# Performance work log

Measured on AMD Instinct MI355X. Metric: run time of the kernel, lower is better.

The kernel has to match this reference:

```python
import jax, jax.numpy as jnp
import numpy as np

L, B, N, D, H = 2, 4, 2048, 1024, 16
DH = D // H
HID = 4 * D
EPS = 1e-5


def setup_inputs() -> dict:
    key = jax.random.key(0)
    ks = jax.random.split(key, 8)
    s = 0.02
    return {
        "tokens": jax.random.normal(ks[0], (B, N, D), jnp.float32),
        "ln1_g": jnp.ones((L, D), jnp.float32),
        "ln1_b": jnp.zeros((L, D), jnp.float32),
        "qkv_w": jax.random.normal(ks[1], (L, 3 * D, D), jnp.float32) * s,
        "qkv_b": jnp.zeros((L, 3 * D), jnp.float32),
        "out_w": jax.random.normal(ks[2], (L, D, D), jnp.float32) * s,
        "out_b": jnp.zeros((L, D), jnp.float32),
        "ln2_g": jnp.ones((L, D), jnp.float32),
        "ln2_b": jnp.zeros((L, D), jnp.float32),
        "fc1_w": jax.random.normal(ks[3], (L, HID, D), jnp.float32) * s,
        "fc1_b": jnp.zeros((L, HID), jnp.float32),
        "fc2_w": jax.random.normal(ks[4], (L, D, HID), jnp.float32) * s,
        "fc2_b": jnp.zeros((L, D), jnp.float32),
    }


def _layernorm(x, g, b):
    mu = jnp.mean(x, axis=-1, keepdims=True)
    var = jnp.mean(jnp.square(x - mu), axis=-1, keepdims=True)
    return (x - mu) * jax.lax.rsqrt(var + EPS) * g + b


def _mha(x, qkv_w, qkv_b, out_w, out_b):
    # nn.MultiheadAttention self-attention, batch_first=True
    qkv = x @ qkv_w.T + qkv_b                        # [B,N,3D]
    q, k, v = jnp.split(qkv, 3, axis=-1)
    q = q.reshape(B, N, H, DH)
    k = k.reshape(B, N, H, DH)
    v = v.reshape(B, N, H, DH)
    scores = jnp.einsum("bqhd,bkhd->bhqk", q, k) / np.sqrt(DH).astype(np.float32)
    attn = jax.nn.softmax(scores, axis=-1)
    o = jnp.einsum("bhqk,bkhd->bqhd", attn, v).reshape(B, N, D)
    return o @ out_w.T + out_b


def reference(tokens, ln1_g, ln1_b, qkv_w, qkv_b, out_w, out_b,
              ln2_g, ln2_b, fc1_w, fc1_b, fc2_w, fc2_b):
    x = tokens
    for i in range(L):
        # NOTE: the original reassigns tokens = norm1(tokens) before residual,
        # so the residual is taken on the NORMED tokens (faithful to source).
        x = _layernorm(x, ln1_g[i], ln1_b[i])
        x = x + _mha(x, qkv_w[i], qkv_b[i], out_w[i], out_b[i])
        x = _layernorm(x, ln2_g[i], ln2_b[i])
        h = jax.nn.gelu(x @ fc1_w[i].T + fc1_b[i], approximate=False)
        x = x + (h @ fc2_w[i].T + fc2_b[i])
    return x  # proj_out / norm_out are Identity since out_dim == dim
```

## Files before the change

kernel.cpp:

```cpp
#include <hip/hip_runtime.h>
#include <cstdint>
#include <cstddef>

typedef unsigned short u16;
typedef __attribute__((ext_vector_type(8))) short bf16x8;
typedef __attribute__((ext_vector_type(8))) u16  u16x8;
typedef __attribute__((ext_vector_type(4))) u16  u16x4;
typedef __attribute__((ext_vector_type(4))) float f32x4;
typedef __attribute__((ext_vector_type(16))) float f32x16;
typedef __attribute__((ext_vector_type(4))) unsigned u32x4;

static __device__ __forceinline__ u16 f2bf(float f) {
  unsigned u = __builtin_bit_cast(unsigned, f);
  u += 0x7fffu + ((u >> 16) & 1u);
  return (u16)(u >> 16);
}
static __device__ __forceinline__ float bf2f(u16 h) {
  return __builtin_bit_cast(float, (unsigned)h << 16);
}
static __device__ __forceinline__ unsigned cvtpk_bf16(float a, float b) {
  unsigned r;
  asm("v_cvt_pk_bf16_f32 %0, %1, %2" : "=v"(r) : "v"(a), "v"(b));
  return r;
}
static __device__ __forceinline__ float rawexp2(float x) {
  float r;
  asm("v_exp_f32 %0, %1" : "=v"(r) : "v"(x));
  return r;
}

static __device__ __forceinline__ void gload16(u16* lds, const u16* g) {
  __builtin_amdgcn_global_load_lds(
      (__attribute__((address_space(1))) unsigned int*)(void*)(g),
      (__attribute__((address_space(3))) unsigned int*)(lds), 16, 0, 0);
}

__global__ __launch_bounds__(256) void cast_f32_bf16(
    const float* __restrict__ s, u16* __restrict__ d, int n4) {
  int i = blockIdx.x * 256 + threadIdx.x;
  if (i < n4) {
    float4 v = ((const float4*)s)[i];
    u16x4 o;
    o[0] = f2bf(v.x); o[1] = f2bf(v.y); o[2] = f2bf(v.z); o[3] = f2bf(v.w);
    ((u16x4*)d)[i] = o;
  }
}

__global__ __launch_bounds__(256) void ln_kernel(
    const float* __restrict__ in, const float* __restrict__ g,
    const float* __restrict__ bb, float* __restrict__ outf,
    u16* __restrict__ outb) {
  const int row = blockIdx.x;
  const int t = threadIdx.x;
  const float4 v = ((const float4*)(in + (size_t)row * 1024))[t];
  float s  = v.x + v.y + v.z + v.w;
  float sq = v.x * v.x + v.y * v.y + v.z * v.z + v.w * v.w;
#pragma unroll
  for (int off = 32; off > 0; off >>= 1) {
    s  += __shfl_down(s, off);
    sq += __shfl_down(sq, off);
  }
  __shared__ float red[8];
  const int w = t >> 6;
  if ((t & 63) == 0) { red[w] = s; red[4 + w] = sq; }
  __syncthreads();
  const float ts  = red[0] + red[1] + red[2] + red[3];
  const float tsq = red[4] + red[5] + red[6] + red[7];
  const float mu = ts * (1.0f / 1024.0f);
  const float rv = rsqrtf(tsq * (1.0f / 1024.0f) - mu * mu + 1e-5f);
  const float4 gv = ((const float4*)g)[t];
  const float4 bv = ((const float4*)bb)[t];
  float4 y;
  y.x = (v.x - mu) * rv * gv.x + bv.x;
  y.y = (v.y - mu) * rv * gv.y + bv.y;
  y.z = (v.z - mu) * rv * gv.z + bv.z;
  y.w = (v.w - mu) * rv * gv.w + bv.w;
  ((float4*)(outf + (size_t)row * 1024))[t] = y;
  u16x4 ob;
  ob[0] = f2bf(y.x); ob[1] = f2bf(y.y); ob[2] = f2bf(y.z); ob[3] = f2bf(y.w);
  *(u16x4*)(outb + (size_t)row * 1024 + t * 4) = ob;
}

#define BM 128
#define BN 128
#define BK 64

template <int MODE>
__global__ __launch_bounds__(256) void gemm_bt(
    const u16* __restrict__ A, const u16* __restrict__ W,
    const float* __restrict__ bias, const float* __restrict__ res,
    u16* __restrict__ outb, float* __restrict__ outf, int Nn, int K) {
  __shared__ u16 As[BM * BK];
  __shared__ u16 Bs[BN * BK];
  const int t  = threadIdx.x;
  const int w  = t >> 6;
  const int ln = t & 63;
  const int lr = ln & 15;
  const int lg = ln >> 4;
  const int bm = blockIdx.x * BM;
  const int bn = blockIdx.y * BN;
  const int wm = (w >> 1) * 64;
  const int wn = (w & 1) * 64;

  f32x4 acc[4][4] = {};

  const int srow = t >> 3;
  const int scol = 8 * ((t & 7) ^ (srow & 7));
  const u16* gA = A + (size_t)(bm + srow) * K + scol;
  const u16* gB = W + (size_t)(bn + srow) * K + scol;
  const char* const AsB = (const char*)As;
  const char* const BsB = (const char*)Bs;

  const int kSteps = K >> 6;
  for (int kt = 0; kt < kSteps; ++kt) {
    __syncthreads();
    const u16* ga = gA + kt * BK;
    const u16* gb = gB + kt * BK;
#pragma unroll
    for (int c = 0; c < 4; ++c) {
      gload16(As + c * 2048 + w * 512, ga + (size_t)(c * 32) * K);
      gload16(Bs + c * 2048 + w * 512, gb + (size_t)(c * 32) * K);
    }
    __syncthreads();

#pragma unroll
    for (int kc = 0; kc < 2; ++kc) {
      bf16x8 af[4], bfr[4];
#pragma unroll
      for (int mi = 0; mi < 4; ++mi) {
        const int row = wm + mi * 16 + lr;
        af[mi] = *(const bf16x8*)(
            AsB + ((row * 128 + kc * 64 + lg * 16) ^ ((row & 7) << 4)));
      }
#pragma unroll
      for (int ni = 0; ni < 4; ++ni) {
        const int row = wn + ni * 16 + lr;
        bfr[ni] = *(const bf16x8*)(
            BsB + ((row * 128 + kc * 64 + lg * 16) ^ ((row & 7) << 4)));
      }
#pragma unroll
      for (int mi = 0; mi < 4; ++mi)
#pragma unroll
        for (int ni = 0; ni < 4; ++ni)
          acc[mi][ni] = __builtin_amdgcn_mfma_f32_16x16x32_bf16(
              af[mi], bfr[ni], acc[mi][ni], 0, 0, 0);
    }
  }

#pragma unroll
  for (int ni = 0; ni < 4; ++ni) {
    const int col = bn + wn + ni * 16 + lr;
    const float bv = bias[col];
#pragma unroll
    for (int mi = 0; mi < 4; ++mi) {
      const int row0 = bm + wm + mi * 16 + lg * 4;
#pragma unroll
      for (int r = 0; r < 4; ++r) {
        float v = acc[mi][ni][r] + bv;
        const size_t idx = (size_t)(row0 + r) * Nn + col;
        if (MODE == 1) v = 0.5f * v * (1.0f + erff(v * 0.70710678118654752f));
        if (MODE == 2) outf[idx] = res[idx] + v;
        else           outb[idx] = f2bf(v);
      }
    }
  }
}

__global__ __launch_bounds__(256, 4) void attn_kernel(
    const u16* __restrict__ qkv, u16* __restrict__ o) {
  __shared__ u16 Ks[2 * 64 * 64];
  __shared__ u16 Vt[2 * 64 * 64];
  const int t   = threadIdx.x;
  const int w   = t >> 6;
  const int l   = t & 63;
  const int q31 = l & 31;
  const int h   = l >> 5;
  const int Lid = blockIdx.x;
  const int v_id = (Lid & 7) * 128 + (Lid >> 3);
  const int bh = v_id >> 4;
  const int b  = bh >> 4;
  const int hd = bh & 15;
  const int qb = (v_id & 15) * 128;
  const size_t baseRow = (size_t)b * 2048;
  const int hcol = hd * 64;

  bf16x8 qf[4];
  {
    const u16* qp = qkv + (baseRow + qb + w * 32 + q31) * 3072 + hcol + h * 8;
    const float qscale = 0.125f * 1.44269504088896f;
#pragma unroll
    for (int f = 0; f < 4; ++f) {
      u16x8 raw = *(const u16x8*)(qp + f * 16);
      bf16x8 q;
#pragma unroll
      for (int i = 0; i < 8; ++i)
        q[i] = (short)f2bf(bf2f(raw[i]) * qscale);
      qf[f] = q;
    }
  }

  f32x16 oacc[2] = {};
  float mrun = -3.0e38f, lrun = 0.0f;

  const int skey = t >> 3;
  const int dK   = 8 * ((t & 7) ^ (skey & 7));
  const int sd0  = (t & 7) * 8;

  {
    gload16(Ks + w * 512,        qkv + (baseRow + skey) * 3072      + 1024 + hcol + dK);
    gload16(Ks + 2048 + w * 512, qkv + (baseRow + 32 + skey) * 3072 + 1024 + hcol + dK);
    u16x8 va = *(const u16x8*)(qkv + (baseRow + skey) * 3072      + 2048 + hcol + sd0);
    u16x8 vb = *(const u16x8*)(qkv + (baseRow + 32 + skey) * 3072 + 2048 + hcol + sd0);
    char* VtB = (char*)Vt;
#pragma unroll
    for (int j = 0; j < 8; ++j) {
      const int sw = (j ^ (t & 7)) << 4;
      *(u16*)(VtB + ((((sd0 + j) * 128 + skey * 2)        ) ^ sw)) = va[j];
      *(u16*)(VtB + ((((sd0 + j) * 128 + (32 + skey) * 2) ) ^ sw)) = vb[j];
    }
  }
  __syncthreads();

  for (int kt = 0; kt < 32; ++kt) {
    char* const KsB = (char*)Ks + (kt & 1) * 8192;
    char* const VtB = (char*)Vt + (kt & 1) * 8192;
    u16* const KsN  = Ks + ((kt & 1) ^ 1) * 4096;
    char* const VtN = (char*)Vt + ((kt & 1) ^ 1) * 8192;

    u16x8 vva, vvb;
    const bool pf = (kt < 31);
    if (pf) {
      const size_t krow = baseRow + (size_t)(kt + 1) * 64;
      gload16(KsN + w * 512,        qkv + (krow + skey) * 3072      + 1024 + hcol + dK);
      gload16(KsN + 2048 + w * 512, qkv + (krow + 32 + skey) * 3072 + 1024 + hcol + dK);
      vva = *(const u16x8*)(qkv + (krow + skey) * 3072      + 2048 + hcol + sd0);
      vvb = *(const u16x8*)(qkv + (krow + 32 + skey) * 3072 + 2048 + hcol + sd0);
    }

    f32x16 s0 = {}, s1 = {};
#pragma unroll
    for (int f = 0; f < 4; ++f) {
      const int d0b = (f * 16 + h * 8) * 2;
      {
        const int row = q31;
        bf16x8 ka = *(const bf16x8*)(KsB + ((row * 128 + d0b) ^ ((row & 7) << 4)));
        s0 = __builtin_amdgcn_mfma_f32_32x32x16_bf16(ka, qf[f], s0, 0, 0, 0);
      }
      {
        const int row = 32 + q31;
        bf16x8 ka = *(const bf16x8*)(KsB + ((row * 128 + d0b) ^ ((row & 7) << 4)));
        s1 = __builtin_amdgcn_mfma_f32_32x32x16_bf16(ka, qf[f], s1, 0, 0, 0);
      }
    }

    float tm[16];
#pragma unroll
    for (int r = 0; r < 16; ++r) tm[r] = fmaxf(s0[r], s1[r]);
#pragma unroll
    for (int st = 8; st >= 1; st >>= 1)
#pragma unroll
      for (int r = 0; r < st; ++r) tm[r] = fmaxf(tm[r], tm[r + st]);
    const float mx = fmaxf(tm[0], __shfl_xor(tm[0], 32));
    const float mn = fmaxf(mrun, mx);
    const float al = rawexp2(mrun - mn);
    mrun = mn;
#pragma unroll
    for (int r = 0; r < 16; ++r) {
      s0[r] = rawexp2(s0[r] - mn);
      s1[r] = rawexp2(s1[r] - mn);
    }
    float tsum[16];
#pragma unroll
    for (int r = 0; r < 16; ++r) tsum[r] = s0[r] + s1[r];
#pragma unroll
    for (int st = 8; st >= 1; st >>= 1)
#pragma unroll
      for (int r = 0; r < st; ++r) tsum[r] += tsum[r + st];
    const float psum = tsum[0] + __shfl_xor(tsum[0], 32);
    lrun = lrun * al + psum;
#pragma unroll
    for (int r = 0; r < 16; ++r) { oacc[0][r] *= al; oacc[1][r] *= al; }

#pragma unroll
    for (int kw = 0; kw < 4; ++kw) {
      const int w1 = kw & 1;
      const f32x16 sv = (kw < 2) ? s0 : s1;
      const unsigned L0 = cvtpk_bf16(sv[8 * w1 + 0], sv[8 * w1 + 1]);
      const unsigned L1 = cvtpk_bf16(sv[8 * w1 + 2], sv[8 * w1 + 3]);
      const unsigned H0 = cvtpk_bf16(sv[8 * w1 + 4], sv[8 * w1 + 5]);
      const unsigned H1 = cvtpk_bf16(sv[8 * w1 + 6], sv[8 * w1 + 7]);
      const unsigned X0 = h ? L0 : H0;
      const unsigned X1 = h ? L1 : H1;
      const unsigned R0 = (unsigned)__shfl_xor((int)X0, 32);
      const unsigned R1 = (unsigned)__shfl_xor((int)X1, 32);
      u32x4 pw;
      pw[0] = h ? R0 : L0;
      pw[1] = h ? R1 : L1;
      pw[2] = h ? H0 : R0;
      pw[3] = h ? H1 : R1;
      const bf16x8 pb = __builtin_bit_cast(bf16x8, pw);
      const int k0b = (kw * 16 + h * 8) * 2;
#pragma unroll
      for (int dt = 0; dt < 2; ++dt) {
        const int d = dt * 32 + q31;
        bf16x8 va = *(const bf16x8*)(
            VtB + ((d * 128 + k0b) ^ ((((d & 7) ^ ((d >> 3) & 7))) << 4)));
        oacc[dt] = __builtin_amdgcn_mfma_f32_32x32x16_bf16(va, pb, oacc[dt], 0, 0, 0);
      }
    }

    if (pf) {
#pragma unroll
      for (int j = 0; j < 8; ++j) {
        const int sw = (j ^ (t & 7)) << 4;
        *(u16*)(VtN + ((((sd0 + j) * 128 + skey * 2)        ) ^ sw)) = vva[j];
        *(u16*)(VtN + ((((sd0 + j) * 128 + (32 + skey) * 2) ) ^ sw)) = vvb[j];
      }
    }
    __syncthreads();
  }

  const float inv = 1.0f / lrun;
  const size_t orow = baseRow + qb + w * 32 + q31;
#pragma unroll
  for (int dt = 0; dt < 2; ++dt)
#pragma unroll
    for (int g = 0; g < 4; ++g) {
      u16x4 ov;
#pragma unroll
      for (int j = 0; j < 4; ++j) ov[j] = f2bf(oacc[dt][g * 4 + j] * inv);
      *(u16x4*)(o + orow * 1024 + hcol + dt * 32 + g * 8 + h * 4) = ov;
    }
}

extern "C" void kernel_launch(void* const* d_in, const int* in_sizes, int n_in,
                              void* d_out, int out_size, void* d_ws,
                              size_t ws_size, hipStream_t stream) {
  const float* tokens = (const float*)d_in[0];
  const float* ln1_g  = (const float*)d_in[1];
  const float* ln1_b  = (const float*)d_in[2];
  const float* qkv_w  = (const float*)d_in[3];
  const float* qkv_b  = (const float*)d_in[4];
  const float* out_w  = (const float*)d_in[5];
  const float* out_b  = (const float*)d_in[6];
  const float* ln2_g  = (const float*)d_in[7];
  const float* ln2_b  = (const float*)d_in[8];
  const float* fc1_w  = (const float*)d_in[9];
  const float* fc1_b  = (const float*)d_in[10];
  const float* fc2_w  = (const float*)d_in[11];
  const float* fc2_b  = (const float*)d_in[12];
  float* xf = (float*)d_out;

  char* ws = (char*)d_ws;
  size_t off = 0;
  auto take = [&](size_t bytes) {
    char* p = ws + off;
    off += (bytes + 255) & ~(size_t)255;
    return p;
  };
  u16* xn    = (u16*)take((size_t)8192 * 1024 * 2);
  u16* big   = (u16*)take((size_t)8192 * 4096 * 2);
  u16* attnb = (u16*)take((size_t)8192 * 1024 * 2);
  u16* qkvw  = (u16*)take((size_t)2 * 3072 * 1024 * 2);
  u16* outw  = (u16*)take((size_t)2 * 1024 * 1024 * 2);
  u16* fc1w  = (u16*)take((size_t)2 * 4096 * 1024 * 2);
  u16* fc2w  = (u16*)take((size_t)2 * 1024 * 4096 * 2);
  u16* qkvb16 = big;
  u16* hb     = big;

  cast_f32_bf16<<<6144, 256, 0, stream>>>(qkv_w, qkvw, 2 * 3072 * 1024 / 4);
  cast_f32_bf16<<<2048, 256, 0, stream>>>(out_w, outw, 2 * 1024 * 1024 / 4);
  cast_f32_bf16<<<8192, 256, 0, stream>>>(fc1_w, fc1w, 2 * 4096 * 1024 / 4);
  cast_f32_bf16<<<8192, 256, 0, stream>>>(fc2_w, fc2w, 2 * 1024 * 4096 / 4);

  for (int i = 0; i < 2; ++i) {
    ln_kernel<<<8192, 256, 0, stream>>>(i == 0 ? tokens : xf,
                                        ln1_g + i * 1024, ln1_b + i * 1024, xf, xn);
    gemm_bt<0><<<dim3(64, 24), 256, 0, stream>>>(
        xn, qkvw + (size_t)i * 3072 * 1024, qkv_b + i * 3072, nullptr,
        qkvb16, nullptr, 3072, 1024);
    attn_kernel<<<1024, 256, 0, stream>>>(qkvb16, attnb);
    gemm_bt<2><<<dim3(64, 8), 256, 0, stream>>>(
        attnb, outw + (size_t)i * 1024 * 1024, out_b + i * 1024, xf,
        nullptr, xf, 1024, 1024);
    ln_kernel<<<8192, 256, 0, stream>>>(xf, ln2_g + i * 1024, ln2_b + i * 1024,
                                        xf, xn);
    gemm_bt<1><<<dim3(64, 32), 256, 0, stream>>>(
        xn, fc1w + (size_t)i * 4096 * 1024, fc1_b + i * 4096, nullptr,
        hb, nullptr, 4096, 1024);
    gemm_bt<2><<<dim3(64, 8), 256, 0, stream>>>(
        hb, fc2w + (size_t)i * 1024 * 4096, fc2_b + i * 1024, xf,
        nullptr, xf, 1024, 4096);
  }
}
```

Baseline: 944.4 us.

## Add lazy softmax rescaling, max3 reduction, and XCD-aware GEMM tile remapping

```diff
diff --git a/kernel.cpp b/kernel.cpp
--- a/kernel.cpp
+++ b/kernel.cpp
@@ -26,6 +26,11 @@
 static __device__ __forceinline__ float rawexp2(float x) {
   float r;
   asm("v_exp_f32 %0, %1" : "=v"(r) : "v"(x));
+  return r;
+}
+static __device__ __forceinline__ float max3f(float a, float b, float c) {
+  float r;
+  asm("v_max3_f32 %0, %1, %2, %3" : "=v"(r) : "v"(a), "v"(b), "v"(c));
   return r;
 }
 
@@ -97,8 +102,11 @@
   const int ln = t & 63;
   const int lr = ln & 15;
   const int lg = ln >> 4;
-  const int bm = blockIdx.x * BM;
-  const int bn = blockIdx.y * BN;
+  const int lin = (int)(blockIdx.y * gridDim.x + blockIdx.x);
+  const int nwg = (int)(gridDim.x * gridDim.y);
+  const int v   = (lin & 7) * (nwg >> 3) + (lin >> 3);
+  const int bm  = (v & 63) * BM;
+  const int bn  = (v >> 6) * BN;
   const int wm = (w >> 1) * 64;
   const int wn = (w & 1) * 64;
 
@@ -156,11 +164,11 @@
       const int row0 = bm + wm + mi * 16 + lg * 4;
 #pragma unroll
       for (int r = 0; r < 4; ++r) {
-        float v = acc[mi][ni][r] + bv;
+        float vv = acc[mi][ni][r] + bv;
         const size_t idx = (size_t)(row0 + r) * Nn + col;
-        if (MODE == 1) v = 0.5f * v * (1.0f + erff(v * 0.70710678118654752f));
-        if (MODE == 2) outf[idx] = res[idx] + v;
-        else           outb[idx] = f2bf(v);
+        if (MODE == 1) vv = 0.5f * vv * (1.0f + erff(vv * 0.70710678118654752f));
+        if (MODE == 2) outf[idx] = res[idx] + vv;
+        else           outb[idx] = f2bf(vv);
       }
     }
   }
@@ -256,18 +264,30 @@
     float tm[16];
 #pragma unroll
     for (int r = 0; r < 16; ++r) tm[r] = fmaxf(s0[r], s1[r]);
-#pragma unroll
-    for (int st = 8; st >= 1; st >>= 1)
-#pragma unroll
-      for (int r = 0; r < st; ++r) tm[r] = fmaxf(tm[r], tm[r + st]);
+    {
+      float a0 = max3f(tm[0], tm[1], tm[2]);
+      float a1 = max3f(tm[3], tm[4], tm[5]);
+      float a2 = max3f(tm[6], tm[7], tm[8]);
+      float a3 = max3f(tm[9], tm[10], tm[11]);
+      float a4 = max3f(tm[12], tm[13], tm[14]);
+      float b0 = max3f(a0, a1, a2);
+      float b1 = max3f(a3, a4, tm[15]);
+      tm[0] = fmaxf(b0, b1);
+    }
     const float mx = fmaxf(tm[0], __shfl_xor(tm[0], 32));
-    const float mn = fmaxf(mrun, mx);
-    const float al = rawexp2(mrun - mn);
-    mrun = mn;
+
+    if (__any(mx > mrun + 8.0f)) {
+      const float mn = fmaxf(mrun, mx);
+      const float al = rawexp2(mrun - mn);
+      mrun = mn;
+      lrun *= al;
+#pragma unroll
+      for (int r = 0; r < 16; ++r) { oacc[0][r] *= al; oacc[1][r] *= al; }
+    }
 #pragma unroll
     for (int r = 0; r < 16; ++r) {
-      s0[r] = rawexp2(s0[r] - mn);
-      s1[r] = rawexp2(s1[r] - mn);
+      s0[r] = rawexp2(s0[r] - mrun);
+      s1[r] = rawexp2(s1[r] - mrun);
     }
     float tsum[16];
 #pragma unroll
@@ -277,9 +297,7 @@
 #pragma unroll
       for (int r = 0; r < st; ++r) tsum[r] += tsum[r + st];
     const float psum = tsum[0] + __shfl_xor(tsum[0], 32);
-    lrun = lrun * al + psum;
-#pragma unroll
-    for (int r = 0; r < 16; ++r) { oacc[0][r] *= al; oacc[1][r] *= al; }
+    lrun += psum;
 
 #pragma unroll
     for (int kw = 0; kw < 4; ++kw) {
```

New measurement: 1.047 ms. 1.11x slower.
